# Kernel tuning notes

Measured on AMD Instinct MI355X. Metric: run time of the kernel, lower is better.

Reference implementation:

```python
import jax, jax.numpy as jnp
import numpy as np

N_SITES = 1024
A_PER_SITE = 2
R_PER_ALLELE = 16
N_ALLELES = N_SITES * A_PER_SITE
N_READS = N_ALLELES * R_PER_ALLELE
C_IN, C, L = 16, 32, 150


def conv1d(x, w, stride=1, dilation=1, pad=2):
    return jax.lax.conv_general_dilated(
        x, w, (stride,), [(pad, pad)], rhs_dilation=(dilation,),
        dimension_numbers=('NCH', 'OIH', 'NCH'))


def reduce_slots(d, slots):
    # cumsum-diff segmented sum over dim 0, exactly as torch reduceSlots
    res = jnp.cumsum(d, axis=0)
    idx = jnp.cumsum(slots) - 1
    sel = res[idx]
    padded = jnp.concatenate([jnp.zeros_like(sel[:1]), sel[:-1]], axis=0)
    return sel - padded


def xattn(allele, site0, site1, wq, wk, wv, wo):
    # cross-attention: allele features query the two expanded site-feature streams
    q = jnp.einsum('oc,ncl->nol', wq, allele)
    kv = jnp.concatenate([site0, site1], axis=-1)  # [Na, C, 2*L']
    k = jnp.einsum('oc,ncl->nol', wk, kv)
    v = jnp.einsum('oc,ncl->nol', wv, kv)
    scores = jnp.einsum('ncl,ncm->nlm', q, k) / np.float32(np.sqrt(C))
    ctx = jnp.einsum('nlm,ncm->ncl', jax.nn.softmax(scores, axis=-1), v)
    return jnp.mean(allele + ctx, axis=-1) @ wo.T  # [Na, 2]


def setup_inputs():
    ks = jax.random.split(jax.random.key(0), 24)
    w = lambda i, shape: jax.random.normal(ks[i], shape, jnp.float32) * 0.05
    return {
        'tensors0': jax.random.normal(ks[0], (N_READS, C_IN, L), jnp.float32),
        'tensors1': jax.random.normal(ks[1], (N_READS, C_IN, L), jnp.float32),
        'conv0_w': w(2, (C, C_IN, 5)), 'conv1_w': w(3, (C, C_IN, 5)),
        'comp0_w': w(4, (C, C, 3)), 'comp1_w': w(5, (C, C, 3)), 'comp2_w': w(6, (C, C, 3)),
        'xq0': w(7, (C, C)), 'xk0': w(8, (C, C)), 'xv0': w(9, (C, C)), 'xo0': w(10, (2, C)),
        'xq1': w(11, (C, C)), 'xk1': w(12, (C, C)), 'xv1': w(13, (C, C)), 'xo1': w(14, (2, C)),
        'xq2': w(15, (C, C)), 'xk2': w(16, (C, C)), 'xv2': w(17, (C, C)), 'xo2': w(18, (2, C)),
        'comb_w': w(19, (C, 2 * C)), 'meta_w': w(20, (3, 2 * C)), 'meta_b': w(21, (3,)),
        'num_alleles_per_site': jnp.full((N_SITES,), A_PER_SITE, jnp.int32),
        'num_reads0': jnp.full((N_ALLELES,), R_PER_ALLELE, jnp.int32),
        'num_reads1': jnp.full((N_ALLELES,), R_PER_ALLELE, jnp.int32),
    }


def reference(tensors0, tensors1, conv0_w, conv1_w, comp0_w, comp1_w, comp2_w,
              xq0, xk0, xv0, xo0, xq1, xk1, xv1, xo1, xq2, xk2, xv2, xo2,
              comb_w, meta_w, meta_b, num_alleles_per_site, num_reads0, num_reads1):
    compressor = lambda x, w: jax.nn.relu(conv1d(x, w, stride=2, dilation=2, pad=2))

    def compress_and_predict(red_allele, comp_w, xw):
        cfa = compressor(red_allele, comp_w)                       # [Na, C, L']
        rfs = reduce_slots(red_allele, num_alleles_per_site)       # [Ns, C, L]
        cfs0 = compressor(rfs, comp_w)                             # [Ns, C, L']
        exp0 = jnp.repeat(cfs0, num_alleles_per_site, axis=0, total_repeat_length=N_ALLELES)
        cfs1 = reduce_slots(cfa, num_alleles_per_site)             # [Ns, C, L']
        exp1 = jnp.repeat(cfs1, num_alleles_per_site, axis=0, total_repeat_length=N_ALLELES)
        return xattn(cfa, exp0, exp1, *xw), (cfs0, cfs1)

    rc0 = jax.nn.relu(conv1d(tensors0, conv0_w, pad=2))            # [Nr, C, L]
    red0 = reduce_slots(rc0, num_reads0)                           # [Na, C, L]
    e0, _ = compress_and_predict(red0, comp0_w, (xq0, xk0, xv0, xo0))

    rc1 = jax.nn.relu(conv1d(tensors1, conv1_w, pad=2))
    red1 = reduce_slots(rc1, num_reads1)
    e1, _ = compress_and_predict(red1, comp1_w, (xq1, xk1, xv1, xo1))

    red2 = jax.nn.relu(jnp.einsum('oc,ncl->nol', comb_w, jnp.concatenate([red0, red1], axis=1)))
    e2, (s0, s1) = compress_and_predict(red2, comp2_w, (xq2, xk2, xv2, xo2))

    meta_feat = jnp.mean(jnp.concatenate([s0, s1], axis=1), axis=-1)  # [Ns, 2C]
    meta = jax.nn.softmax(meta_feat @ meta_w.T + meta_b, axis=-1)     # [Ns, 3]
    return (jnp.stack([e0, e1, e2]), meta)
```

## Files before the change

kernel.cpp:

```cpp
#include <hip/hip_runtime.h>
#include <math.h>

#define NS 1024
#define NA 2048
#define CIN 16
#define CC 32
#define LL 150
#define LC 75

typedef __attribute__((ext_vector_type(8))) short short8;
typedef __attribute__((ext_vector_type(4))) float float4v;

__device__ __forceinline__ unsigned short f2bf(float f) {
  unsigned int u = __float_as_uint(f);
  unsigned int r = (u + 0x7FFFu + ((u >> 16) & 1u)) >> 16;
  return (unsigned short)r;
}

__device__ __forceinline__ unsigned int pkbf(float lo, float hi) {
  return (unsigned int)f2bf(lo) | ((unsigned int)f2bf(hi) << 16);
}

__global__ __launch_bounds__(256) void k_conv_sum_mfma(const float* __restrict__ x,
                                                       const float* __restrict__ w,
                                                       float* __restrict__ red) {
  __shared__ unsigned short xs[2][154 * 32];
  const int a = blockIdx.x;
  const int tid = threadIdx.x;
  const int lane = tid & 63;
  const int wv = tid >> 6;

  short8 afr[2][3];
  {
    const int mrow = lane & 15;
    const int h = lane >> 4;
    for (int mt = 0; mt < 2; ++mt) {
      const int c = mt * 16 + mrow;
      for (int s = 0; s < 3; ++s) {
        short8 f;
#pragma unroll
        for (int j = 0; j < 8; ++j) {
          int ic = 4 * h + (j >> 1);
          int tap = 2 * s + (j & 1);
          float wval = (tap < 5) ? w[c * 80 + ic * 5 + tap] : 0.f;
          f[j] = (short)f2bf(wval);
        }
        afr[mt][s] = f;
      }
    }
  }

  float4v sum[2][3];
#pragma unroll
  for (int mt = 0; mt < 2; ++mt)
#pragma unroll
    for (int nt = 0; nt < 3; ++nt) sum[mt][nt] = (float4v)(0.f);

  const int nbase = wv * 48;
  const int nrow = lane & 15;
  const int hh = lane >> 4;
  const float4v zf = (float4v)(0.f);

  auto stage = [&](int r, int buf) {
    const float* xr = x + (size_t)(a * 16 + r) * (CIN * LL);
    unsigned int* xb32 = (unsigned int*)xs[buf];
    for (int idx = tid; idx < 16 * 38; idx += 256) {
      const int ic = idx & 15;
      const int seg = idx >> 4;
      const int l0 = seg * 4;
      const float* row = xr + ic * LL;
      float v0, v1, v2, v3, v4;
      if (seg < 37) {
        float2 u = *(const float2*)(row + l0);
        float2 u2 = *(const float2*)(row + l0 + 2);
        v0 = u.x; v1 = u.y; v2 = u2.x; v3 = u2.y;
        v4 = row[l0 + 4];
      } else {
        float2 u = *(const float2*)(row + 148);
        v0 = u.x; v1 = u.y; v2 = 0.f; v3 = 0.f; v4 = 0.f;
      }
      const int hb = 4 * (ic >> 2) + (ic & 3);
      unsigned int* b32 = xb32 + 16 * (l0 + 2) + hb;
      b32[0]  = pkbf(v0, v1);
      b32[16] = pkbf(v1, v2);
      b32[32] = pkbf(v2, v3);
      b32[48] = pkbf(v3, v4);
    }
    if (tid < 32) {
      const int ic = tid & 15;
      const int which = tid >> 4;
      const int hb = 4 * (ic >> 2) + (ic & 3);
      xb32[16 * which + hb] = which ? pkbf(0.f, xr[ic * LL]) : 0u;
    }
  };

  stage(0, 0);
  __syncthreads();

  for (int r = 0; r < 16; ++r) {
    const int cur = r & 1;
    if (r + 1 < 16) stage(r + 1, cur ^ 1);

    float4v acc[2][3];
#pragma unroll
    for (int s = 0; s < 3; ++s) {
#pragma unroll
      for (int nt = 0; nt < 3; ++nt) {
        int p = nbase + nt * 16 + nrow + 2 * s;
        if (p >= 154) p -= 154;
        short8 bfrag = *(const short8*)&xs[cur][(4 * p + hh) * 8];
#pragma unroll
        for (int mt = 0; mt < 2; ++mt) {
          acc[mt][nt] = __builtin_amdgcn_mfma_f32_16x16x32_bf16(
              afr[mt][s], bfrag, (s == 0) ? zf : acc[mt][nt], 0, 0, 0);
        }
      }
    }
#pragma unroll
    for (int mt = 0; mt < 2; ++mt)
#pragma unroll
      for (int nt = 0; nt < 3; ++nt)
#pragma unroll
        for (int q = 0; q < 4; ++q) sum[mt][nt][q] += fmaxf(acc[mt][nt][q], 0.f);

    __syncthreads();
  }

  const int ccol = lane & 15;
  const int crow4 = (lane >> 4) * 4;
  for (int mt = 0; mt < 2; ++mt)
    for (int nt = 0; nt < 3; ++nt) {
      int l = nbase + nt * 16 + ccol;
      if (l < LL) {
#pragma unroll
        for (int q = 0; q < 4; ++q) {
          int c = mt * 16 + crow4 + q;
          red[(size_t)a * (CC * LL) + c * LL + l] = sum[mt][nt][q];
        }
      }
    }
}

__global__ __launch_bounds__(256) void k_comb(const float* __restrict__ red0,
                                              const float* __restrict__ red1,
                                              const float* __restrict__ cw,
                                              float* __restrict__ out) {
  __shared__ float ins[64][152];
  __shared__ float cwl[64][CC];
  const int a = blockIdx.x;
  const int tid = threadIdx.x;

  for (int i = tid; i < 64 * CC; i += 256) {
    int c = i & 31; int c2 = i >> 5;
    cwl[c2][c] = cw[c * 64 + c2];
  }
  for (int i = tid; i < CC * LL; i += 256) {
    int c2 = i / LL; int l = i - c2 * LL;
    ins[c2][l] = red0[(size_t)a * (CC * LL) + i];
    ins[32 + c2][l] = red1[(size_t)a * (CC * LL) + i];
  }
  __syncthreads();

  const int c = tid & 31;
  const int lg = tid >> 5;
  const int l0 = lg * 19;
  const int nl = (LL - l0 < 19) ? (LL - l0) : 19;
  float v[19];
#pragma unroll
  for (int j = 0; j < 19; ++j) v[j] = 0.f;
  for (int c2 = 0; c2 < 64; ++c2) {
    float wv = cwl[c2][c];
#pragma unroll
    for (int j = 0; j < 19; ++j) v[j] += wv * ins[c2][l0 + j];
  }
  float* o = out + (size_t)a * (CC * LL) + c * LL + l0;
  for (int j = 0; j < nl; ++j) o[j] = fmaxf(v[j], 0.f);
}

#define BKV   0
#define BWK   4800
#define BWV   5856
#define BWQ   6912
#define BQT   7968
#define BCF   10368
#define BKB   10368
#define BVB   15232
#define BROWP 0
#define BPART 6080
#define BMS   6592
#define ARENA 20224
#define FIN0  0
#define FIN1  5248
#define FWS   10496

__device__ __forceinline__ void attn_phase_d(float* __restrict__ ar, int g, int t,
                                             float& ms) {
  const float scale = 0.17677669529663687f;
  const int rbase = BROWP + g * 760;
#pragma unroll 1
  for (int cc = 0; cc < 2; ++cc) {
    const int ch = g + 8 * cc;
    if (ch >= 15) break;
    const int r0 = ch * 5;

    float2 acc[5][3];
#pragma unroll
    for (int i = 0; i < 5; ++i)
#pragma unroll
      for (int u = 0; u < 3; ++u) acc[i][u] = make_float2(0.f, 0.f);

#pragma unroll 1
    for (int c2 = 0; c2 < 32; c2 += 2) {
      float2 q01[5];
#pragma unroll
      for (int i = 0; i < 5; ++i) q01[i] = *(const float2*)&ar[BQT + (r0 + i) * 32 + c2];
      const int cb0 = BKB + c2 * 152 + 2 * t;
      const int cb1 = cb0 + 152;
      float2 ka0 = *(const float2*)&ar[cb0];
      float2 ka1 = *(const float2*)&ar[cb0 + 64];
      float2 ka2 = *(const float2*)&ar[cb0 + 128];
      float2 kb0 = *(const float2*)&ar[cb1];
      float2 kb1 = *(const float2*)&ar[cb1 + 64];
      float2 kb2 = *(const float2*)&ar[cb1 + 128];
#pragma unroll
      for (int i = 0; i < 5; ++i) {
        acc[i][0].x += q01[i].x * ka0.x + q01[i].y * kb0.x;
        acc[i][0].y += q01[i].x * ka0.y + q01[i].y * kb0.y;
        acc[i][1].x += q01[i].x * ka1.x + q01[i].y * kb1.x;
        acc[i][1].y += q01[i].x * ka1.y + q01[i].y * kb1.y;
        acc[i][2].x += q01[i].x * ka2.x + q01[i].y * kb2.x;
        acc[i][2].y += q01[i].x * ka2.y + q01[i].y * kb2.y;
      }
    }

    float inv[5];
#pragma unroll
    for (int i = 0; i < 5; ++i) {
      float s0x = acc[i][0].x * scale, s0y = acc[i][0].y * scale;
      float s1x = acc[i][1].x * scale, s1y = acc[i][1].y * scale;
      float s2x = acc[i][2].x * scale, s2y = acc[i][2].y * scale;
      if (t >= 11) { s2x = -1e30f; s2y = -1e30f; }
      float mx = fmaxf(fmaxf(fmaxf(s0x, s0y), fmaxf(s1x, s1y)), fmaxf(s2x, s2y));
#pragma unroll
      for (int off = 16; off > 0; off >>= 1) mx = fmaxf(mx, __shfl_xor(mx, off, 32));
      float p0x = __expf(s0x - mx), p0y = __expf(s0y - mx);
      float p1x = __expf(s1x - mx), p1y = __expf(s1y - mx);
      float p2x = __expf(s2x - mx), p2y = __expf(s2y - mx);
      float ss = p0x + p0y + p1x + p1y + p2x + p2y;
#pragma unroll
      for (int off = 16; off > 0; off >>= 1) ss += __shfl_xor(ss, off, 32);
      inv[i] = 1.f / ss;
      const int rb = rbase + i * 152 + 2 * t;
      *(float2*)&ar[rb]      = make_float2(p0x, p0y);
      *(float2*)&ar[rb + 64] = make_float2(p1x, p1y);
      if (t <= 11) *(float2*)&ar[rb + 128] = make_float2(p2x, p2y);
    }

    float pv[5] = {0.f, 0.f, 0.f, 0.f, 0.f};
    for (int mq = 0; mq < 38; ++mq) {
      float4 vv = *(const float4*)&ar[BVB + t * 156 + 4 * mq];
#pragma unroll
      for (int i = 0; i < 5; ++i) {
        float4 pp = *(const float4*)&ar[rbase + i * 152 + 4 * mq];
        pv[i] += pp.x * vv.x + pp.y * vv.y + pp.z * vv.z + pp.w * vv.w;
      }
    }
#pragma unroll
    for (int i = 0; i < 5; ++i) ms += pv[i] * inv[i];
  }
}

__global__ __launch_bounds__(256) void k_cattn(const float* __restrict__ red,
                                               const float* __restrict__ cw,
                                               const float* __restrict__ wq,
                                               const float* __restrict__ wk,
                                               const float* __restrict__ wv,
                                               const float* __restrict__ wo,
                                               float* __restrict__ cfa,
                                               float* __restrict__ cfs,
                                               float* __restrict__ eout,
                                               int wg) {
  __shared__ float ar[ARENA];
  const int s = blockIdx.x;
  const int tid = threadIdx.x;
  const int g = tid >> 5;
  const int t = tid & 31;

  float* a0g = cfa + (size_t)(2 * s) * (CC * LC);
  float* a1g = a0g + CC * LC;
  float* sgw = cfs + (size_t)s * (CC * LC);

  for (int i = tid; i < CC * 3 * CC; i += 256) {
    int c = i & 31; int kk = i >> 5;
    ar[FWS + kk * 32 + c] = cw[c * (CC * 3) + kk];
  }
  if (tid < CC) {
    ar[FIN0 + tid * 164 + 0] = 0.f; ar[FIN0 + tid * 164 + 1] = 0.f;
    ar[FIN0 + tid * 164 + 152] = 0.f; ar[FIN0 + tid * 164 + 153] = 0.f;
    ar[FIN1 + tid * 164 + 0] = 0.f; ar[FIN1 + tid * 164 + 1] = 0.f;
    ar[FIN1 + tid * 164 + 152] = 0.f; ar[FIN1 + tid * 164 + 153] = 0.f;
  }
  {
    const float* s0 = red + (size_t)(2 * s) * (CC * LL);
    const float* s1 = s0 + CC * LL;
    for (int i = tid; i < CC * LL; i += 256) {
      int ic = i / LL; int l = i - ic * LL;
      ar[FIN0 + ic * 164 + l + 2] = s0[i];
      ar[FIN1 + ic * 164 + l + 2] = s1[i];
    }
  }
  __syncthreads();

  const int j0 = g * 10;
  const int nj = (LC - j0 < 10) ? (LC - j0) : 10;
  float v0[10], v1[10];
#pragma unroll
  for (int j = 0; j < 10; ++j) { v0[j] = 0.f; v1[j] = 0.f; }
  for (int ic = 0; ic < CC; ++ic) {
    float w0 = ar[FWS + (ic * 3 + 0) * 32 + t];
    float w1 = ar[FWS + (ic * 3 + 1) * 32 + t];
    float w2 = ar[FWS + (ic * 3 + 2) * 32 + t];
    float xa[12], xb[12];
#pragma unroll
    for (int i = 0; i < 12; ++i) {
      xa[i] = ar[FIN0 + ic * 164 + 2 * j0 + 2 * i];
      xb[i] = ar[FIN1 + ic * 164 + 2 * j0 + 2 * i];
    }
#pragma unroll
    for (int j = 0; j < 10; ++j) {
      v0[j] += w0 * xa[j] + w1 * xa[j + 1] + w2 * xa[j + 2];
      v1[j] += w0 * xb[j] + w1 * xb[j + 1] + w2 * xb[j + 2];
    }
  }
  __syncthreads();

  for (int j = 0; j < nj; ++j) {
    const int jj = j0 + j;
    float r0 = fmaxf(v0[j], 0.f);
    float r1 = fmaxf(v1[j], 0.f);
    float cs = fmaxf(v0[j] + v1[j], 0.f);
    ar[BKV + t * 150 + jj]      = cs;
    ar[BKV + t * 150 + 75 + jj] = r0 + r1;
    ar[BCF + t * 77 + jj]       = r0;
    a1g[t * 75 + jj] = r1;
    if (wg) {
      a0g[t * 75 + jj] = r0;
      sgw[t * 75 + jj] = cs;
    }
  }
  for (int i = tid; i < CC * CC; i += 256) {
    int o = i >> 5, ii = i & 31;
    ar[BWQ + ii * 33 + o] = wq[i];
    ar[BWK + ii * 33 + o] = wk[i];
    ar[BWV + ii * 33 + o] = wv[i];
  }
  __syncthreads();

  float cfp0 = 0.f;
  {
    float wqc[32];
#pragma unroll
    for (int ii = 0; ii < 32; ++ii) wqc[ii] = ar[BWQ + ii * 33 + t];
    for (int row = g; row < 75; row += 8) {
      float acc = 0.f;
#pragma unroll
      for (int ii = 0; ii < 32; ++ii) acc += wqc[ii] * ar[BCF + ii * 77 + row];
      ar[BQT + row * 32 + t] = acc;
      cfp0 += ar[BCF + t * 77 + row];
    }
  }
  __syncthreads();

  {
    float wkc[32], wvc[32];
#pragma unroll
    for (int ii = 0; ii < 32; ++ii) {
      wkc[ii] = ar[BWK + ii * 33 + t];
      wvc[ii] = ar[BWV + ii * 33 + t];
    }
    for (int idx = tid; idx < CC * LL; idx += 256) {
      int o = idx & 31, m = idx >> 5;
      float ka = 0.f, va = 0.f;
#pragma unroll
      for (int ii = 0; ii < 32; ++ii) {
        float x = ar[BKV + ii * 150 + m];
        ka += wkc[ii] * x;
        va += wvc[ii] * x;
      }
      ar[BKB + o * 152 + m] = ka;
      ar[BVB + o * 156 + m] = va;
    }
    if (tid < 64) ar[BVB + (tid >> 1) * 156 + 150 + (tid & 1)] = 0.f;
  }
  __syncthreads();

  float ms0 = 0.f;
  attn_phase_d(ar, g, t, ms0);
  __syncthreads();

  float cfp1 = 0.f;
  {
    float wqc[32];
#pragma unroll
    for (int ii = 0; ii < 32; ++ii) wqc[ii] = ar[BWQ + ii * 33 + t];
    for (int row = g; row < 75; row += 8) {
      float acc = 0.f;
#pragma unroll
      for (int ii = 0; ii < 32; ++ii) acc += wqc[ii] * a1g[ii * 75 + row];
      ar[BQT + row * 32 + t] = acc;
      cfp1 += a1g[t * 75 + row];
    }
  }
  __syncthreads();

  float ms1 = 0.f;
  attn_phase_d(ar, g, t, ms1);

  ar[BPART + g * 32 + t]       = cfp0 + ms0;
  ar[BPART + 256 + g * 32 + t] = cfp1 + ms1;
  __syncthreads();

  if (tid < 64) {
    int al = tid >> 5, tt = tid & 31;
    float tot = 0.f;
#pragma unroll
    for (int gg = 0; gg < 8; ++gg) tot += ar[BPART + al * 256 + gg * 32 + tt];
    ar[BMS + al * 32 + tt] = tot * (1.f / 75.f);
  }
  __syncthreads();
  if (tid < 4) {
    int al = tid >> 1, o2 = tid & 1;
    float e = 0.f;
#pragma unroll
    for (int c2 = 0; c2 < CC; ++c2) e += wo[o2 * CC + c2] * ar[BMS + al * 32 + c2];
    eout[s * 4 + tid] = e;
  }
}

__global__ __launch_bounds__(64) void k_meta(const float* __restrict__ cfs0,
                                             const float* __restrict__ cfa2,
                                             const float* __restrict__ mw,
                                             const float* __restrict__ mb,
                                             float* __restrict__ mout) {
  __shared__ float feat[64];
  __shared__ float lgt[3];
  const int s = blockIdx.x;
  const int tid = threadIdx.x;
  float f = 0.f;
  if (tid < 32) {
    const float* p = cfs0 + (size_t)s * (CC * LC) + tid * LC;
    for (int l = 0; l < LC; ++l) f += p[l];
  } else {
    const float* p0 = cfa2 + (size_t)(2 * s) * (CC * LC) + (tid - 32) * LC;
    const float* p1 = cfa2 + (size_t)(2 * s + 1) * (CC * LC) + (tid - 32) * LC;
    for (int l = 0; l < LC; ++l) f += p0[l] + p1[l];
  }
  feat[tid] = f * (1.f / 75.f);
  __syncthreads();
  if (tid < 3) {
    float acc2 = mb[tid];
    for (int c2 = 0; c2 < 64; ++c2) acc2 += mw[tid * 64 + c2] * feat[c2];
    lgt[tid] = acc2;
  }
  __syncthreads();
  if (tid < 3) {
    float mx = fmaxf(lgt[0], fmaxf(lgt[1], lgt[2]));
    float e0 = __expf(lgt[0] - mx), e1 = __expf(lgt[1] - mx), e2 = __expf(lgt[2] - mx);
    mout[s * 3 + tid] = __expf(lgt[tid] - mx) / (e0 + e1 + e2);
  }
}

extern "C" void kernel_launch(void* const* d_in, const int* in_sizes, int n_in,
                              void* d_out, int out_size, void* d_ws, size_t ws_size,
                              hipStream_t stream) {
  const float* t0      = (const float*)d_in[0];
  const float* t1      = (const float*)d_in[1];
  const float* conv0_w = (const float*)d_in[2];
  const float* conv1_w = (const float*)d_in[3];
  const float* comp0_w = (const float*)d_in[4];
  const float* comp1_w = (const float*)d_in[5];
  const float* comp2_w = (const float*)d_in[6];
  const float* xq0 = (const float*)d_in[7];
  const float* xk0 = (const float*)d_in[8];
  const float* xv0 = (const float*)d_in[9];
  const float* xo0 = (const float*)d_in[10];
  const float* xq1 = (const float*)d_in[11];
  const float* xk1 = (const float*)d_in[12];
  const float* xv1 = (const float*)d_in[13];
  const float* xo1 = (const float*)d_in[14];
  const float* xq2 = (const float*)d_in[15];
  const float* xk2 = (const float*)d_in[16];
  const float* xv2 = (const float*)d_in[17];
  const float* xo2 = (const float*)d_in[18];
  const float* comb_w = (const float*)d_in[19];
  const float* meta_w = (const float*)d_in[20];
  const float* meta_b = (const float*)d_in[21];

  float* wsf  = (float*)d_ws;
  float* red0 = wsf;
  float* red1 = red0 + (size_t)NA * CC * LL;
  float* cfa  = red1 + (size_t)NA * CC * LL;
  float* cfs0 = cfa + (size_t)NA * CC * LC;
  float* out  = (float*)d_out;

  k_conv_sum_mfma<<<NA, 256, 0, stream>>>(t0, conv0_w, red0);
  k_conv_sum_mfma<<<NA, 256, 0, stream>>>(t1, conv1_w, red1);

  k_cattn<<<NS, 256, 0, stream>>>(red0, comp0_w, xq0, xk0, xv0, xo0,
                                  cfa, cfs0, out + 0, 0);
  k_cattn<<<NS, 256, 0, stream>>>(red1, comp1_w, xq1, xk1, xv1, xo1,
                                  cfa, cfs0, out + 2 * NA, 0);

  k_comb<<<NA, 256, 0, stream>>>(red0, red1, comb_w, red0);
  k_cattn<<<NS, 256, 0, stream>>>(red0, comp2_w, xq2, xk2, xv2, xo2,
                                  cfa, cfs0, out + 4 * NA, 1);

  k_meta<<<NS, 64, 0, stream>>>(cfs0, cfa, meta_w, meta_b, out + 6 * NA);
}
```

Before: 1.361 ms.

## Store attention K/V/probabilities in bf16 LDS and use bf16 dot2

```diff
diff --git a/kernel.cpp b/kernel.cpp
--- a/kernel.cpp
+++ b/kernel.cpp
@@ -20,6 +20,21 @@
 __device__ __forceinline__ unsigned int pkbf(float lo, float hi) {
   return (unsigned int)f2bf(lo) | ((unsigned int)f2bf(hi) << 16);
 }
+
+__device__ __forceinline__ float bflo(unsigned int u) { return __uint_as_float(u << 16); }
+__device__ __forceinline__ float bfhi(unsigned int u) { return __uint_as_float(u & 0xffff0000u); }
+
+#if __has_builtin(__builtin_amdgcn_fdot2_f32_bf16)
+typedef __attribute__((ext_vector_type(2))) __bf16 bf16x2;
+__device__ __forceinline__ float bdot2(unsigned int a, unsigned int b, float c) {
+  return __builtin_amdgcn_fdot2_f32_bf16(__builtin_bit_cast(bf16x2, a),
+                                         __builtin_bit_cast(bf16x2, b), c, false);
+}
+#else
+__device__ __forceinline__ float bdot2(unsigned int a, unsigned int b, float c) {
+  return c + bflo(a) * bflo(b) + bfhi(a) * bfhi(b);
+}
+#endif
 
 __global__ __launch_bounds__(256) void k_conv_sum_mfma(const float* __restrict__ x,
                                                        const float* __restrict__ w,
@@ -177,26 +192,25 @@
   for (int j = 0; j < nl; ++j) o[j] = fmaxf(v[j], 0.f);
 }
 
-#define BKV   0
-#define BWK   4800
-#define BWV   5856
-#define BWQ   6912
-#define BQT   7968
-#define BCF   10368
-#define BKB   10368
-#define BVB   15232
-#define BROWP 0
-#define BPART 6080
-#define BMS   6592
-#define ARENA 20224
+#define BWK   2400
+#define BWV   3456
+#define BWQ   4512
+#define BQT   5568
+#define BCF   7968
+#define KB_US 15936
+#define VB_US 20864
+#define BPART 3456
+#define BMS   3968
+#define ARENA 13056
 #define FIN0  0
-#define FIN1  5248
-#define FWS   10496
+#define FIN1  4992
+#define FWS   9984
 
 __device__ __forceinline__ void attn_phase_d(float* __restrict__ ar, int g, int t,
                                              float& ms) {
+  unsigned short* aru = (unsigned short*)ar;
   const float scale = 0.17677669529663687f;
-  const int rbase = BROWP + g * 760;
+  const int rb_us = g * 760;
 #pragma unroll 1
   for (int cc = 0; cc < 2; ++cc) {
     const int ch = g + 8 * cc;
@@ -214,22 +228,28 @@
       float2 q01[5];
 #pragma unroll
       for (int i = 0; i < 5; ++i) q01[i] = *(const float2*)&ar[BQT + (r0 + i) * 32 + c2];
-      const int cb0 = BKB + c2 * 152 + 2 * t;
-      const int cb1 = cb0 + 152;
-      float2 ka0 = *(const float2*)&ar[cb0];
-      float2 ka1 = *(const float2*)&ar[cb0 + 64];
-      float2 ka2 = *(const float2*)&ar[cb0 + 128];
-      float2 kb0 = *(const float2*)&ar[cb1];
-      float2 kb1 = *(const float2*)&ar[cb1 + 64];
-      float2 kb2 = *(const float2*)&ar[cb1 + 128];
+      const int k0 = KB_US + c2 * 154 + 2 * t;
+      const int k1 = k0 + 154;
+      unsigned int a0 = *(const unsigned int*)&aru[k0];
+      unsigned int a1 = *(const unsigned int*)&aru[k0 + 64];
+      unsigned int a2 = *(const unsigned int*)&aru[k0 + 128];
+      unsigned int b0 = *(const unsigned int*)&aru[k1];
+      unsigned int b1 = *(const unsigned int*)&aru[k1 + 64];
+      unsigned int b2 = *(const unsigned int*)&aru[k1 + 128];
+      float ka0x = bflo(a0), ka0y = bfhi(a0);
+      float ka1x = bflo(a1), ka1y = bfhi(a1);
+      float ka2x = bflo(a2), ka2y = bfhi(a2);
+      float kb0x = bflo(b0), kb0y = bfhi(b0);
+      float kb1x = bflo(b1), kb1y = bfhi(b1);
+      float kb2x = bflo(b2), kb2y = bfhi(b2);
 #pragma unroll
       for (int i = 0; i < 5; ++i) {
-        acc[i][0].x += q01[i].x * ka0.x + q01[i].y * kb0.x;
-        acc[i][0].y += q01[i].x * ka0.y + q01[i].y * kb0.y;
-        acc[i][1].x += q01[i].x * ka1.x + q01[i].y * kb1.x;
-        acc[i][1].y += q01[i].x * ka1.y + q01[i].y * kb1.y;
-        acc[i][2].x += q01[i].x * ka2.x + q01[i].y * kb2.x;
-        acc[i][2].y += q01[i].x * ka2.y + q01[i].y * kb2.y;
+        acc[i][0].x += q01[i].x * ka0x + q01[i].y * kb0x;
+        acc[i][0].y += q01[i].x * ka0y + q01[i].y * kb0y;
+        acc[i][1].x += q01[i].x * ka1x + q01[i].y * kb1x;
+        acc[i][1].y += q01[i].x * ka1y + q01[i].y * kb1y;
+        acc[i][2].x += q01[i].x * ka2x + q01[i].y * kb2x;
+        acc[i][2].y += q01[i].x * ka2y + q01[i].y * kb2y;
       }
     }
 
@@ -250,19 +270,21 @@
 #pragma unroll
       for (int off = 16; off > 0; off >>= 1) ss += __shfl_xor(ss, off, 32);
       inv[i] = 1.f / ss;
-      const int rb = rbase + i * 152 + 2 * t;
-      *(float2*)&ar[rb]      = make_float2(p0x, p0y);
-      *(float2*)&ar[rb + 64] = make_float2(p1x, p1y);
-      if (t <= 11) *(float2*)&ar[rb + 128] = make_float2(p2x, p2y);
+      const int rw = rb_us + i * 152 + 2 * t;
+      *(unsigned int*)&aru[rw]      = pkbf(p0x, p0y);
+      *(unsigned int*)&aru[rw + 64] = pkbf(p1x, p1y);
+      if (t <= 11) *(unsigned int*)&aru[rw + 128] = pkbf(p2x, p2y);
     }
 
     float pv[5] = {0.f, 0.f, 0.f, 0.f, 0.f};
+    const int vb = VB_US + t * 164;
     for (int mq = 0; mq < 38; ++mq) {
-      float4 vv = *(const float4*)&ar[BVB + t * 156 + 4 * mq];
+      uint2 vv = *(const uint2*)&aru[vb + 4 * mq];
 #pragma unroll
       for (int i = 0; i < 5; ++i) {
-        float4 pp = *(const float4*)&ar[rbase + i * 152 + 4 * mq];
-        pv[i] += pp.x * vv.x + pp.y * vv.y + pp.z * vv.z + pp.w * vv.w;
+        uint2 pp = *(const uint2*)&aru[rb_us + i * 152 + 4 * mq];
+        pv[i] = bdot2(pp.x, vv.x, pv[i]);
+        pv[i] = bdot2(pp.y, vv.y, pv[i]);
       }
     }
 #pragma unroll
@@ -281,6 +303,7 @@
                                                float* __restrict__ eout,
                                                int wg) {
   __shared__ float ar[ARENA];
+  unsigned short* aru = (unsigned short*)ar;
   const int s = blockIdx.x;
   const int tid = threadIdx.x;
   const int g = tid >> 5;
@@ -295,18 +318,18 @@
     ar[FWS + kk * 32 + c] = cw[c * (CC * 3) + kk];
   }
   if (tid < CC) {
-    ar[FIN0 + tid * 164 + 0] = 0.f; ar[FIN0 + tid * 164 + 1] = 0.f;
-    ar[FIN0 + tid * 164 + 152] = 0.f; ar[FIN0 + tid * 164 + 153] = 0.f;
-    ar[FIN1 + tid * 164 + 0] = 0.f; ar[FIN1 + tid * 164 + 1] = 0.f;
-    ar[FIN1 + tid * 164 + 152] = 0.f; ar[FIN1 + tid * 164 + 153] = 0.f;
+    ar[FIN0 + tid * 156 + 0] = 0.f; ar[FIN0 + tid * 156 + 1] = 0.f;
+    ar[FIN0 + tid * 156 + 152] = 0.f; ar[FIN0 + tid * 156 + 153] = 0.f;
+    ar[FIN1 + tid * 156 + 0] = 0.f; ar[FIN1 + tid * 156 + 1] = 0.f;
+    ar[FIN1 + tid * 156 + 152] = 0.f; ar[FIN1 + tid * 156 + 153] = 0.f;
   }
   {
     const float* s0 = red + (size_t)(2 * s) * (CC * LL);
     const float* s1 = s0 + CC * LL;
     for (int i = tid; i < CC * LL; i += 256) {
       int ic = i / LL; int l = i - ic * LL;
-      ar[FIN0 + ic * 164 + l + 2] = s0[i];
-      ar[FIN1 + ic * 164 + l + 2] = s1[i];
+      ar[FIN0 + ic * 156 + l + 2] = s0[i];
+      ar[FIN1 + ic * 156 + l + 2] = s1[i];
     }
   }
   __syncthreads();
@@ -323,8 +346,8 @@
     float xa[12], xb[12];
 #pragma unroll
     for (int i = 0; i < 12; ++i) {
-      xa[i] = ar[FIN0 + ic * 164 + 2 * j0 + 2 * i];
-      xb[i] = ar[FIN1 + ic * 164 + 2 * j0 + 2 * i];
+      xa[i] = ar[FIN0 + ic * 156 + 2 * j0 + 2 * i];
+      xb[i] = ar[FIN1 + ic * 156 + 2 * j0 + 2 * i];
     }
 #pragma unroll
     for (int j = 0; j < 10; ++j) {
@@ -339,9 +362,9 @@
     float r0 = fmaxf(v0[j], 0.f);
     float r1 = fmaxf(v1[j], 0.f);
     float cs = fmaxf(v0[j] + v1[j], 0.f);
-    ar[BKV + t * 150 + jj]      = cs;
-    ar[BKV + t * 150 + 75 + jj] = r0 + r1;
-    ar[BCF + t * 77 + jj]       = r0;
+    aru[jj * 32 + t]        = f2bf(cs);
+    aru[(75 + jj) * 32 + t] = f2bf(r0 + r1);
+    ar[BCF + t * 77 + jj]   = r0;
     a1g[t * 75 + jj] = r1;
     if (wg) {
       a0g[t * 75 + jj] = r0;
@@ -372,25 +395,34 @@
   __syncthreads();
 
   {
-    float wkc[32], wvc[32];
-#pragma unroll
-    for (int ii = 0; ii < 32; ++ii) {
-      wkc[ii] = ar[BWK + ii * 33 + t];
-      wvc[ii] = ar[BWV + ii * 33 + t];
+    unsigned int wk2[16], wv2[16];
+    {
+      float wkc[32], wvc[32];
+#pragma unroll
+      for (int ii = 0; ii < 32; ++ii) {
+        wkc[ii] = ar[BWK + ii * 33 + t];
+        wvc[ii] = ar[BWV + ii * 33 + t];
+      }
+#pragma unroll
+      for (int j = 0; j < 16; ++j) {
+        wk2[j] = pkbf(wkc[2 * j], wkc[2 * j + 1]);
+        wv2[j] = pkbf(wvc[2 * j], wvc[2 * j + 1]);
+      }
     }
     for (int idx = tid; idx < CC * LL; idx += 256) {
       int o = idx & 31, m = idx >> 5;
+      const unsigned int* kvrow = (const unsigned int*)&aru[m * 32];
       float ka = 0.f, va = 0.f;
 #pragma unroll
-      for (int ii = 0; ii < 32; ++ii) {
-        float x = ar[BKV + ii * 150 + m];
-        ka += wkc[ii] * x;
-        va += wvc[ii] * x;
-      }
-      ar[BKB + o * 152 + m] = ka;
-      ar[BVB + o * 156 + m] = va;
-    }
-    if (tid < 64) ar[BVB + (tid >> 1) * 156 + 150 + (tid & 1)] = 0.f;
+      for (int j = 0; j < 16; ++j) {
+        unsigned int u = kvrow[j];
+        ka = bdot2(wk2[j], u, ka);
+        va = bdot2(wv2[j], u, va);
+      }
+      aru[KB_US + o * 154 + m] = f2bf(ka);
+      aru[VB_US + o * 164 + m] = f2bf(va);
+    }
+    if (tid < 32) *(unsigned int*)&aru[VB_US + tid * 164 + 150] = 0u;
   }
   __syncthreads();
 
```

Measured after the change: 1.231 ms. -9.5%, faster.
